# Performance work log

Hardware: AMD Instinct MI355X
Metric: run time of the kernel (lower is better)

## Reference

```python
import jax, jax.numpy as jnp
import numpy as np

N_NODES = 100000
N_EDGES = 1600000
F_NODE = 32
F_EDGE = 32
HID = 64
N_TGT = 32


def setup_inputs() -> dict:
    key = jax.random.key(0)
    ks = jax.random.split(key, 12)
    x = jax.random.normal(ks[0], (N_NODES, F_NODE), dtype=jnp.float32)
    edge_index = jax.random.randint(ks[1], (2, N_EDGES), 0, N_NODES, dtype=jnp.int64)
    edge_attr = jax.random.normal(ks[2], (N_EDGES, F_EDGE), dtype=jnp.float32)
    u = jax.random.normal(ks[3], (1, 8), dtype=jnp.float32)
    batch = jnp.zeros((N_NODES,), dtype=jnp.int64)
    s1 = 1.0 / np.sqrt(F_NODE + F_EDGE)
    s2 = 1.0 / np.sqrt(HID)
    s3 = 1.0 / np.sqrt(HID + F_NODE)
    W1a = jax.random.uniform(ks[4], (F_NODE + F_EDGE, HID), jnp.float32, -s1, s1)
    b1a = jax.random.uniform(ks[5], (HID,), jnp.float32, -s1, s1)
    W1b = jax.random.uniform(ks[6], (HID, HID), jnp.float32, -s2, s2)
    b1b = jax.random.uniform(ks[7], (HID,), jnp.float32, -s2, s2)
    W2a = jax.random.uniform(ks[8], (HID + F_NODE, HID), jnp.float32, -s3, s3)
    b2a = jax.random.uniform(ks[9], (HID,), jnp.float32, -s3, s3)
    W2b = jax.random.uniform(ks[10], (HID, N_TGT), jnp.float32, -s2, s2)
    b2b = jax.random.uniform(ks[11], (N_TGT,), jnp.float32, -s2, s2)
    return {"x": x, "edge_index": edge_index, "edge_attr": edge_attr, "u": u,
            "batch": batch, "W1a": W1a, "b1a": b1a, "W1b": W1b, "b1b": b1b,
            "W2a": W2a, "b2a": b2a, "W2b": W2b, "b2b": b2b}


def reference(x, edge_index, edge_attr, u, batch,
              W1a, b1a, W1b, b1b, W2a, b2a, W2b, b2b):
    row, col = edge_index[0], edge_index[1]
    n = x.shape[0]
    # gather source node features and concat with edge features -> edge MLP
    m = jnp.concatenate([x[col], edge_attr], axis=1)           # [E, F_NODE+F_EDGE]
    m = jax.nn.relu(m @ W1a + b1a) @ W1b + b1b                  # [E, HID]
    # scatter-mean back to destination nodes (row)
    summed = jax.ops.segment_sum(m, row, num_segments=n)        # [N, HID]
    counts = jax.ops.segment_sum(jnp.ones((m.shape[0],), m.dtype), row, num_segments=n)
    agg = summed / jnp.maximum(counts, 1.0)[:, None]
    h = jnp.concatenate([x, agg], axis=1)                       # [N, HID+F_NODE]
    out = jax.nn.relu(h @ W2a + b2a) @ W2b + b2b                # [N, N_TGT]
    return out
```

## Files before the change

kernel.cpp:

```cpp
#include <hip/hip_runtime.h>

#define NN 100000
#define NE 1600000
#define NB ((NN + 255) / 256)

typedef unsigned int uint32;
typedef unsigned short ushort16;
typedef float f32x4 __attribute__((ext_vector_type(4)));
typedef short bf16x8 __attribute__((ext_vector_type(8)));

__device__ __forceinline__ float bflo(uint32 u) { return __uint_as_float(u << 16); }
__device__ __forceinline__ float bfhi(uint32 u) { return __uint_as_float(u & 0xffff0000u); }
__device__ __forceinline__ uint32 bfbits(float v) { return (__float_as_uint(v) + 0x8000u) >> 16; }
__device__ __forceinline__ uint32 pack2(float a, float b) { return bfbits(a) | (bfbits(b) << 16); }

__device__ __forceinline__ int sigma_ch(int c) {
    return (((c >> 2) & 3) << 4) + (((c >> 4) & 3) << 2) + (c & 3);
}

__global__ __launch_bounds__(256) void k_hist_rank(const int* __restrict__ ei, int* __restrict__ deg,
                                                   int* __restrict__ rank, int E) {
    int e = blockIdx.x * 256 + threadIdx.x;
    if (e < E) rank[e] = atomicAdd(&deg[ei[e]], 1);
}

__global__ __launch_bounds__(256) void k_hist(const int* __restrict__ ei, int* __restrict__ deg, int E) {
    int e = blockIdx.x * 256 + threadIdx.x;
    if (e < E) atomicAdd(&deg[ei[e]], 1);
}

__global__ __launch_bounds__(256) void k_scan1(const int* __restrict__ deg, int* __restrict__ offs,
                                               int* __restrict__ bsums, int n) {
    __shared__ int s[256];
    int tid = threadIdx.x;
    int i = blockIdx.x * 256 + tid;
    int v = (i < n) ? deg[i] : 0;
    int acc = v;
    s[tid] = acc;
    __syncthreads();
    #pragma unroll
    for (int off = 1; off < 256; off <<= 1) {
        int t = (tid >= off) ? s[tid - off] : 0;
        __syncthreads();
        acc += t;
        s[tid] = acc;
        __syncthreads();
    }
    if (i < n) offs[i] = acc - v;
    if (tid == 255) bsums[blockIdx.x] = acc;
}

__global__ __launch_bounds__(512) void k_scan2(int* __restrict__ bsums, int nb) {
    __shared__ int s[512];
    int tid = threadIdx.x;
    int v = (tid < nb) ? bsums[tid] : 0;
    int acc = v;
    s[tid] = acc;
    __syncthreads();
    #pragma unroll
    for (int off = 1; off < 512; off <<= 1) {
        int t = (tid >= off) ? s[tid - off] : 0;
        __syncthreads();
        acc += t;
        s[tid] = acc;
        __syncthreads();
    }
    bsums[tid] = acc - v;
}

__global__ __launch_bounds__(256) void k_offs(int* __restrict__ offs, const int* __restrict__ bsums, int n) {
    int i = blockIdx.x * 256 + threadIdx.x;
    if (i < n) offs[i] += bsums[i >> 8];
}

__global__ __launch_bounds__(256) void k_sorted(const int* __restrict__ ei, const int* __restrict__ offs,
                                                const int* __restrict__ rank, int* __restrict__ sorted, int E) {
    int e = blockIdx.x * 256 + threadIdx.x;
    if (e >= E) return;
    sorted[offs[ei[e]] + rank[e]] = e;
}

__global__ __launch_bounds__(256) void k_prep(const float* __restrict__ W1b, const float* __restrict__ b1b,
                                              const float* __restrict__ W2a,
                                              float* __restrict__ Wc, float* __restrict__ bc, int perm) {
    int t = blockIdx.x * 256 + threadIdx.x;
    int r = t >> 6, c = t & 63;
    float a = 0.f;
    for (int k = 0; k < 64; ++k) a += W1b[r * 64 + k] * W2a[(32 + k) * 64 + c];
    int rs = perm ? sigma_ch(r) : r;
    Wc[rs * 64 + c] = a;
    if (t < 64) {
        float bacc = 0.f;
        for (int k = 0; k < 64; ++k) bacc += b1b[k] * W2a[(32 + k) * 64 + t];
        bc[t] = bacc;
    }
}

__global__ __launch_bounds__(256) void k_edge_fused(
    const int* __restrict__ ei, const float* __restrict__ ea, const float* __restrict__ x,
    const float* __restrict__ W1a, const float* __restrict__ b1a,
    const int* __restrict__ deg, const int* __restrict__ offs, const int* __restrict__ sorted,
    float* __restrict__ Sacc)
{
    __shared__ ushort16 sWtB[64 * 40];
    __shared__ ushort16 sWtA[64 * 40];
    for (int idx = threadIdx.x; idx < 2048; idx += 256) {
        int ch = idx & 63, k = idx >> 6;
        sWtB[ch * 40 + k] = (ushort16)bfbits(W1a[(32 + k) * 64 + ch]);
        sWtA[ch * 40 + k] = (ushort16)bfbits(W1a[k * 64 + ch]);
    }
    __syncthreads();

    int lane = threadIdx.x & 63;
    int wave = threadIdx.x >> 6;
    int en = lane & 15;
    int qq = lane >> 4;
    int node = blockIdx.x * 4 + wave;
    if (node >= NN) return;

    bf16x8 wB[4], wA[4];
    #pragma unroll
    for (int cc = 0; cc < 4; ++cc) {
        wB[cc] = *(const bf16x8*)&sWtB[(cc * 16 + en) * 40 + qq * 8];
        wA[cc] = *(const bf16x8*)&sWtA[(cc * 16 + en) * 40 + qq * 8];
    }
    f32x4 binit[4];
    #pragma unroll
    for (int cc = 0; cc < 4; ++cc) {
        float4 b = *(const float4*)(b1a + cc * 16 + qq * 4);
        binit[cc] = (f32x4){b.x, b.y, b.z, b.w};
    }

    int d = deg[node];
    int start = offs[node];

    f32x4 tot[4];
    #pragma unroll
    for (int cc = 0; cc < 4; ++cc) tot[cc] = (f32x4){0.f, 0.f, 0.f, 0.f};

    #pragma unroll 1
    for (int t0 = 0; t0 < d; t0 += 16) {
        int sidx = t0 + en;
        bool ok = sidx < d;
        union { uint4 u; bf16x8 v; } bea, bx;
        f32x4 acc[4];
        if (ok) {
            int e = sorted[start + sidx];
            int col = ei[NE + e];
            const float* ar = ea + (size_t)e * 32 + qq * 8;
            float4 a0 = *(const float4*)ar;
            float4 a1 = *(const float4*)(ar + 4);
            bea.u.x = pack2(a0.x, a0.y); bea.u.y = pack2(a0.z, a0.w);
            bea.u.z = pack2(a1.x, a1.y); bea.u.w = pack2(a1.z, a1.w);
            const float* xr = x + (size_t)col * 32 + qq * 8;
            float4 x0 = *(const float4*)xr;
            float4 x1 = *(const float4*)(xr + 4);
            bx.u.x = pack2(x0.x, x0.y); bx.u.y = pack2(x0.z, x0.w);
            bx.u.z = pack2(x1.x, x1.y); bx.u.w = pack2(x1.z, x1.w);
            #pragma unroll
            for (int cc = 0; cc < 4; ++cc) acc[cc] = binit[cc];
        } else {
            bea.u = make_uint4(0, 0, 0, 0);
            bx.u = make_uint4(0, 0, 0, 0);
            #pragma unroll
            for (int cc = 0; cc < 4; ++cc) acc[cc] = (f32x4){0.f, 0.f, 0.f, 0.f};
        }
        #pragma unroll
        for (int cc = 0; cc < 4; ++cc)
            acc[cc] = __builtin_amdgcn_mfma_f32_16x16x32_bf16(wB[cc], bea.v, acc[cc], 0, 0, 0);
        #pragma unroll
        for (int cc = 0; cc < 4; ++cc)
            acc[cc] = __builtin_amdgcn_mfma_f32_16x16x32_bf16(wA[cc], bx.v, acc[cc], 0, 0, 0);
        #pragma unroll
        for (int cc = 0; cc < 4; ++cc) {
            #pragma unroll
            for (int r = 0; r < 4; ++r)
                tot[cc][r] += fmaxf(acc[cc][r], 0.f);
        }
    }

    #pragma unroll
    for (int m = 1; m < 16; m <<= 1) {
        #pragma unroll
        for (int cc = 0; cc < 4; ++cc) {
            #pragma unroll
            for (int r = 0; r < 4; ++r)
                tot[cc][r] += __shfl_xor(tot[cc][r], m);
        }
    }
    if (en == 0) {
        float* sp = Sacc + (size_t)node * 64 + qq * 16;
        #pragma unroll
        for (int cc = 0; cc < 4; ++cc)
            *(float4*)(sp + cc * 4) = make_float4(tot[cc][0], tot[cc][1], tot[cc][2], tot[cc][3]);
    }
}

__global__ __launch_bounds__(256) void k_edge_atom(
    const float* __restrict__ x, const int* __restrict__ ei, const float* __restrict__ ea,
    const float* __restrict__ W1a, const float* __restrict__ b1a,
    float* __restrict__ Sacc, int E)
{
    __shared__ float sWB[32 * 64];
    __shared__ float sWA[32 * 64];
    __shared__ float sb[64];
    for (int t = threadIdx.x; t < 32 * 64; t += 256) {
        sWB[t] = W1a[32 * 64 + t];
        sWA[t] = W1a[t];
    }
    if (threadIdx.x < 64) sb[threadIdx.x] = b1a[threadIdx.x];
    __syncthreads();
    int e = blockIdx.x * 256 + threadIdx.x;
    if (e >= E) return;
    int row = ei[e];
    int col = ei[NE + e];
    float h[64];
    #pragma unroll
    for (int j = 0; j < 64; ++j) h[j] = sb[j];
    const float4* xrow = (const float4*)(x + (size_t)col * 32);
    #pragma unroll
    for (int k4 = 0; k4 < 8; ++k4) {
        float4 v = xrow[k4];
        float vv[4] = {v.x, v.y, v.z, v.w};
        #pragma unroll
        for (int c = 0; c < 4; ++c) {
            float val = vv[c];
            const float4* wr = (const float4*)&sWA[(k4 * 4 + c) * 64];
            #pragma unroll
            for (int j4 = 0; j4 < 16; ++j4) {
                float4 w = wr[j4];
                h[j4 * 4 + 0] += val * w.x; h[j4 * 4 + 1] += val * w.y;
                h[j4 * 4 + 2] += val * w.z; h[j4 * 4 + 3] += val * w.w;
            }
        }
    }
    const float4* earow = (const float4*)(ea + (size_t)e * 32);
    #pragma unroll
    for (int k4 = 0; k4 < 8; ++k4) {
        float4 v = earow[k4];
        float vv[4] = {v.x, v.y, v.z, v.w};
        #pragma unroll
        for (int c = 0; c < 4; ++c) {
            float val = vv[c];
            const float4* wr = (const float4*)&sWB[(k4 * 4 + c) * 64];
            #pragma unroll
            for (int j4 = 0; j4 < 16; ++j4) {
                float4 w = wr[j4];
                h[j4 * 4 + 0] += val * w.x; h[j4 * 4 + 1] += val * w.y;
                h[j4 * 4 + 2] += val * w.z; h[j4 * 4 + 3] += val * w.w;
            }
        }
    }
    float* srow = Sacc + (size_t)row * 64;
    #pragma unroll
    for (int j = 0; j < 64; ++j) atomicAdd(&srow[j], fmaxf(h[j], 0.f));
}

__global__ __launch_bounds__(256) void k_node(
    const float* __restrict__ x, const float* __restrict__ Sacc, const int* __restrict__ deg,
    const float* __restrict__ Wc, const float* __restrict__ bc,
    const float* __restrict__ W2a, const float* __restrict__ b2a,
    const float* __restrict__ W2b, const float* __restrict__ b2b,
    float* __restrict__ out, int N)
{
    __shared__ float sWc[64 * 64];
    __shared__ float sW2ax[32 * 64];
    __shared__ float sW2b[64 * 32];
    __shared__ float sbc2[64];
    __shared__ float sb2[64];
    __shared__ float sb2b_[32];
    for (int t = threadIdx.x; t < 64 * 64; t += 256) sWc[t] = Wc[t];
    for (int t = threadIdx.x; t < 32 * 64; t += 256) sW2ax[t] = W2a[t];
    for (int t = threadIdx.x; t < 64 * 32; t += 256) sW2b[t] = W2b[t];
    if (threadIdx.x < 64) {
        sbc2[threadIdx.x] = bc[threadIdx.x] + b2a[threadIdx.x];
        sb2[threadIdx.x] = b2a[threadIdx.x];
    }
    if (threadIdx.x < 32) sb2b_[threadIdx.x] = b2b[threadIdx.x];
    __syncthreads();

    int i = blockIdx.x * 256 + threadIdx.x;
    if (i >= N) return;
    int d = deg[i];
    float inv = (d > 0) ? 1.f / (float)d : 0.f;

    float h2[64];
    #pragma unroll
    for (int j = 0; j < 64; ++j) h2[j] = (d > 0) ? sbc2[j] : sb2[j];

    const float4* sp = (const float4*)(Sacc + (size_t)i * 64);
    #pragma unroll 2
    for (int k4 = 0; k4 < 16; ++k4) {
        float4 v = sp[k4];
        float vv[4] = {v.x * inv, v.y * inv, v.z * inv, v.w * inv};
        #pragma unroll
        for (int c = 0; c < 4; ++c) {
            float val = vv[c];
            const float4* wr = (const float4*)&sWc[(k4 * 4 + c) * 64];
            #pragma unroll
            for (int j4 = 0; j4 < 16; ++j4) {
                float4 w = wr[j4];
                h2[j4 * 4 + 0] += val * w.x; h2[j4 * 4 + 1] += val * w.y;
                h2[j4 * 4 + 2] += val * w.z; h2[j4 * 4 + 3] += val * w.w;
            }
        }
    }
    const float4* xrow = (const float4*)(x + (size_t)i * 32);
    #pragma unroll 2
    for (int k4 = 0; k4 < 8; ++k4) {
        float4 v = xrow[k4];
        float vv[4] = {v.x, v.y, v.z, v.w};
        #pragma unroll
        for (int c = 0; c < 4; ++c) {
            float val = vv[c];
            const float4* wr = (const float4*)&sW2ax[(k4 * 4 + c) * 64];
            #pragma unroll
            for (int j4 = 0; j4 < 16; ++j4) {
                float4 w = wr[j4];
                h2[j4 * 4 + 0] += val * w.x; h2[j4 * 4 + 1] += val * w.y;
                h2[j4 * 4 + 2] += val * w.z; h2[j4 * 4 + 3] += val * w.w;
            }
        }
    }
    #pragma unroll
    for (int j = 0; j < 64; ++j) h2[j] = fmaxf(h2[j], 0.f);

    float o[32];
    #pragma unroll
    for (int j = 0; j < 32; ++j) o[j] = sb2b_[j];
    #pragma unroll
    for (int k = 0; k < 64; ++k) {
        float val = h2[k];
        const float4* wr = (const float4*)&sW2b[k * 32];
        #pragma unroll
        for (int j4 = 0; j4 < 8; ++j4) {
            float4 w = wr[j4];
            o[j4 * 4 + 0] += val * w.x; o[j4 * 4 + 1] += val * w.y;
            o[j4 * 4 + 2] += val * w.z; o[j4 * 4 + 3] += val * w.w;
        }
    }
    float4* orow = (float4*)(out + (size_t)i * 32);
    #pragma unroll
    for (int q = 0; q < 8; ++q)
        orow[q] = make_float4(o[q * 4], o[q * 4 + 1], o[q * 4 + 2], o[q * 4 + 3]);
}

extern "C" void kernel_launch(void* const* d_in, const int* in_sizes, int n_in,
                              void* d_out, int out_size, void* d_ws, size_t ws_size,
                              hipStream_t stream) {
    const float* x   = (const float*)d_in[0];
    const int*   ei  = (const int*)d_in[1];
    const float* ea  = (const float*)d_in[2];
    const float* W1a = (const float*)d_in[5];
    const float* b1a = (const float*)d_in[6];
    const float* W1b = (const float*)d_in[7];
    const float* b1b = (const float*)d_in[8];
    const float* W2a = (const float*)d_in[9];
    const float* b2a = (const float*)d_in[10];
    const float* W2b = (const float*)d_in[11];
    const float* b2b = (const float*)d_in[12];
    float* out = (float*)d_out;

    char* p = (char*)d_ws;
    int* deg        = (int*)p;        p += (size_t)NN * 4;
    int* offs       = (int*)p;        p += (size_t)NN * 4;
    int* bsums      = (int*)p;        p += 2048;
    float* Wc       = (float*)p;      p += 4096 * 4;
    float* bc       = (float*)p;      p += 64 * 4;
    int* rank       = (int*)p;        p += (size_t)NE * 4;
    int* sorted     = (int*)p;        p += (size_t)NE * 4;
    float* Sacc     = (float*)p;      p += (size_t)NN * 64 * 4;
    size_t need     = (size_t)(p - (char*)d_ws);

    dim3 blk(256);
    bool primary = (ws_size >= need);

    if (primary) {
        hipMemsetAsync(deg, 0, (size_t)NN * 4, stream);
        hipLaunchKernelGGL(k_hist_rank, dim3((NE + 255) / 256), blk, 0, stream, ei, deg, rank, NE);
        hipLaunchKernelGGL(k_scan1, dim3(NB), blk, 0, stream, deg, offs, bsums, NN);
        hipLaunchKernelGGL(k_scan2, dim3(1), dim3(512), 0, stream, bsums, NB);
        hipLaunchKernelGGL(k_offs, dim3(NB), blk, 0, stream, offs, bsums, NN);
        hipLaunchKernelGGL(k_sorted, dim3((NE + 255) / 256), blk, 0, stream, ei, offs, rank, sorted, NE);
        hipLaunchKernelGGL(k_prep, dim3(16), blk, 0, stream, W1b, b1b, W2a, Wc, bc, 1);
        hipLaunchKernelGGL(k_edge_fused, dim3((NN + 3) / 4), blk, 0, stream,
                           ei, ea, x, W1a, b1a, deg, offs, sorted, Sacc);
        hipLaunchKernelGGL(k_node, dim3(NB), blk, 0, stream,
                           x, Sacc, deg, Wc, bc, W2a, b2a, W2b, b2b, out, NN);
    } else {
        hipMemsetAsync(deg, 0, (size_t)NN * 4, stream);
        hipMemsetAsync(Sacc, 0, (size_t)NN * 64 * 4, stream);
        hipLaunchKernelGGL(k_hist, dim3((NE + 255) / 256), blk, 0, stream, ei, deg, NE);
        hipLaunchKernelGGL(k_prep, dim3(16), blk, 0, stream, W1b, b1b, W2a, Wc, bc, 0);
        hipLaunchKernelGGL(k_edge_atom, dim3((NE + 255) / 256), blk, 0, stream,
                           x, ei, ea, W1a, b1a, Sacc, NE);
        hipLaunchKernelGGL(k_node, dim3(NB), blk, 0, stream,
                           x, Sacc, deg, Wc, bc, W2a, b2a, W2b, b2b, out, NN);
    }
}
```

Before: 333.0 us.

## Store edge id with source col during sort and prepack W1a MFMA fragments

The sort kernel now writes an (edge id, source column) pair per sorted slot, so the edge kernel no longer does a dependent gather of ei to find the column. W1a is converted to bf16 once in k_prep, stored in MFMA fragment layout, and loaded straight into registers. This drops the per-block shared-memory staging loop and its barrier. Out-of-range lanes now load a clamped valid slot, so loads are issued unconditionally. The trade-offs are a sorted array twice as large to write and read, and extra redundant loads for masked lanes.

Result: faster. 313.4 us (-5.9%).

```diff
diff --git a/kernel.cpp b/kernel.cpp
--- a/kernel.cpp
+++ b/kernel.cpp
@@ -74,15 +74,17 @@
 }
 
 __global__ __launch_bounds__(256) void k_sorted(const int* __restrict__ ei, const int* __restrict__ offs,
-                                                const int* __restrict__ rank, int* __restrict__ sorted, int E) {
+                                                const int* __restrict__ rank, int2* __restrict__ ecol, int E) {
     int e = blockIdx.x * 256 + threadIdx.x;
     if (e >= E) return;
-    sorted[offs[ei[e]] + rank[e]] = e;
+    int slot = offs[ei[e]] + rank[e];
+    ecol[slot] = make_int2(e, ei[E + e]);
 }
 
 __global__ __launch_bounds__(256) void k_prep(const float* __restrict__ W1b, const float* __restrict__ b1b,
-                                              const float* __restrict__ W2a,
-                                              float* __restrict__ Wc, float* __restrict__ bc, int perm) {
+                                              const float* __restrict__ W2a, const float* __restrict__ W1a,
+                                              float* __restrict__ Wc, float* __restrict__ bc,
+                                              uint4* __restrict__ wpack, int perm) {
     int t = blockIdx.x * 256 + threadIdx.x;
     int r = t >> 6, c = t & 63;
     float a = 0.f;
@@ -94,23 +96,29 @@
         for (int k = 0; k < 64; ++k) bacc += b1b[k] * W2a[(32 + k) * 64 + t];
         bc[t] = bacc;
     }
+    if (t < 512) {
+        int table = t >> 8;
+        int cc = (t >> 6) & 3;
+        int lane = t & 63;
+        int qq = lane >> 4, en = lane & 15;
+        int ch = cc * 16 + en;
+        uint32 w[4];
+        #pragma unroll
+        for (int j = 0; j < 4; ++j) {
+            int k0 = qq * 8 + j * 2;
+            int row0 = (table ? 0 : 32) + k0;
+            w[j] = pack2(W1a[row0 * 64 + ch], W1a[(row0 + 1) * 64 + ch]);
+        }
+        wpack[t] = make_uint4(w[0], w[1], w[2], w[3]);
+    }
 }
 
 __global__ __launch_bounds__(256) void k_edge_fused(
-    const int* __restrict__ ei, const float* __restrict__ ea, const float* __restrict__ x,
-    const float* __restrict__ W1a, const float* __restrict__ b1a,
-    const int* __restrict__ deg, const int* __restrict__ offs, const int* __restrict__ sorted,
+    const float* __restrict__ ea, const float* __restrict__ x,
+    const uint4* __restrict__ wpack, const float* __restrict__ b1a,
+    const int* __restrict__ deg, const int* __restrict__ offs, const int2* __restrict__ ecol,
     float* __restrict__ Sacc)
 {
-    __shared__ ushort16 sWtB[64 * 40];
-    __shared__ ushort16 sWtA[64 * 40];
-    for (int idx = threadIdx.x; idx < 2048; idx += 256) {
-        int ch = idx & 63, k = idx >> 6;
-        sWtB[ch * 40 + k] = (ushort16)bfbits(W1a[(32 + k) * 64 + ch]);
-        sWtA[ch * 40 + k] = (ushort16)bfbits(W1a[k * 64 + ch]);
-    }
-    __syncthreads();
-
     int lane = threadIdx.x & 63;
     int wave = threadIdx.x >> 6;
     int en = lane & 15;
@@ -118,11 +126,11 @@
     int node = blockIdx.x * 4 + wave;
     if (node >= NN) return;
 
-    bf16x8 wB[4], wA[4];
+    union { uint4 u; bf16x8 v; } wB[4], wA[4];
     #pragma unroll
     for (int cc = 0; cc < 4; ++cc) {
-        wB[cc] = *(const bf16x8*)&sWtB[(cc * 16 + en) * 40 + qq * 8];
-        wA[cc] = *(const bf16x8*)&sWtA[(cc * 16 + en) * 40 + qq * 8];
+        wB[cc].u = wpack[cc * 64 + lane];
+        wA[cc].u = wpack[256 + cc * 64 + lane];
     }
     f32x4 binit[4];
     #pragma unroll
@@ -142,19 +150,21 @@
     for (int t0 = 0; t0 < d; t0 += 16) {
         int sidx = t0 + en;
         bool ok = sidx < d;
+        int slot = start + (ok ? sidx : d - 1);
+        int2 ec = ecol[slot];
+
+        const float* ar = ea + (size_t)ec.x * 32 + qq * 8;
+        float4 a0 = *(const float4*)ar;
+        float4 a1 = *(const float4*)(ar + 4);
+        const float* xr = x + (size_t)ec.y * 32 + qq * 8;
+        float4 x0 = *(const float4*)xr;
+        float4 x1 = *(const float4*)(xr + 4);
+
         union { uint4 u; bf16x8 v; } bea, bx;
         f32x4 acc[4];
         if (ok) {
-            int e = sorted[start + sidx];
-            int col = ei[NE + e];
-            const float* ar = ea + (size_t)e * 32 + qq * 8;
-            float4 a0 = *(const float4*)ar;
-            float4 a1 = *(const float4*)(ar + 4);
             bea.u.x = pack2(a0.x, a0.y); bea.u.y = pack2(a0.z, a0.w);
             bea.u.z = pack2(a1.x, a1.y); bea.u.w = pack2(a1.z, a1.w);
-            const float* xr = x + (size_t)col * 32 + qq * 8;
-            float4 x0 = *(const float4*)xr;
-            float4 x1 = *(const float4*)(xr + 4);
             bx.u.x = pack2(x0.x, x0.y); bx.u.y = pack2(x0.z, x0.w);
             bx.u.z = pack2(x1.x, x1.y); bx.u.w = pack2(x1.z, x1.w);
             #pragma unroll
@@ -167,10 +177,10 @@
         }
         #pragma unroll
         for (int cc = 0; cc < 4; ++cc)
-            acc[cc] = __builtin_amdgcn_mfma_f32_16x16x32_bf16(wB[cc], bea.v, acc[cc], 0, 0, 0);
+            acc[cc] = __builtin_amdgcn_mfma_f32_16x16x32_bf16(wB[cc].v, bea.v, acc[cc], 0, 0, 0);
         #pragma unroll
         for (int cc = 0; cc < 4; ++cc)
-            acc[cc] = __builtin_amdgcn_mfma_f32_16x16x32_bf16(wA[cc], bx.v, acc[cc], 0, 0, 0);
+            acc[cc] = __builtin_amdgcn_mfma_f32_16x16x32_bf16(wA[cc].v, bx.v, acc[cc], 0, 0, 0);
         #pragma unroll
         for (int cc = 0; cc < 4; ++cc) {
             #pragma unroll
@@ -367,34 +377,36 @@
     int* bsums      = (int*)p;        p += 2048;
     float* Wc       = (float*)p;      p += 4096 * 4;
     float* bc       = (float*)p;      p += 64 * 4;
+    uint4* wpack    = (uint4*)p;      p += 512 * 16;
+    size_t off_fb   = (size_t)(p - (char*)d_ws);
     int* rank       = (int*)p;        p += (size_t)NE * 4;
-    int* sorted     = (int*)p;        p += (size_t)NE * 4;
+    int2* ecol      = (int2*)p;       p += (size_t)NE * 8;
     float* Sacc     = (float*)p;      p += (size_t)NN * 64 * 4;
     size_t need     = (size_t)(p - (char*)d_ws);
 
     dim3 blk(256);
-    bool primary = (ws_size >= need);
-
-    if (primary) {
+
+    if (ws_size >= need) {
         hipMemsetAsync(deg, 0, (size_t)NN * 4, stream);
         hipLaunchKernelGGL(k_hist_rank, dim3((NE + 255) / 256), blk, 0, stream, ei, deg, rank, NE);
         hipLaunchKernelGGL(k_scan1, dim3(NB), blk, 0, stream, deg, offs, bsums, NN);
         hipLaunchKernelGGL(k_scan2, dim3(1), dim3(512), 0, stream, bsums, NB);
         hipLaunchKernelGGL(k_offs, dim3(NB), blk, 0, stream, offs, bsums, NN);
-        hipLaunchKernelGGL(k_sorted, dim3((NE + 255) / 256), blk, 0, stream, ei, offs, rank, sorted, NE);
-        hipLaunchKernelGGL(k_prep, dim3(16), blk, 0, stream, W1b, b1b, W2a, Wc, bc, 1);
+        hipLaunchKernelGGL(k_sorted, dim3((NE + 255) / 256), blk, 0, stream, ei, offs, rank, ecol, NE);
+        hipLaunchKernelGGL(k_prep, dim3(16), blk, 0, stream, W1b, b1b, W2a, W1a, Wc, bc, wpack, 1);
         hipLaunchKernelGGL(k_edge_fused, dim3((NN + 3) / 4), blk, 0, stream,
-                           ei, ea, x, W1a, b1a, deg, offs, sorted, Sacc);
+                           ea, x, wpack, b1a, deg, offs, ecol, Sacc);
         hipLaunchKernelGGL(k_node, dim3(NB), blk, 0, stream,
                            x, Sacc, deg, Wc, bc, W2a, b2a, W2b, b2b, out, NN);
     } else {
+        float* Sacc_fb = (float*)((char*)d_ws + off_fb);
         hipMemsetAsync(deg, 0, (size_t)NN * 4, stream);
-        hipMemsetAsync(Sacc, 0, (size_t)NN * 64 * 4, stream);
+        hipMemsetAsync(Sacc_fb, 0, (size_t)NN * 64 * 4, stream);
         hipLaunchKernelGGL(k_hist, dim3((NE + 255) / 256), blk, 0, stream, ei, deg, NE);
-        hipLaunchKernelGGL(k_prep, dim3(16), blk, 0, stream, W1b, b1b, W2a, Wc, bc, 0);
+        hipLaunchKernelGGL(k_prep, dim3(16), blk, 0, stream, W1b, b1b, W2a, W1a, Wc, bc, wpack, 0);
         hipLaunchKernelGGL(k_edge_atom, dim3((NE + 255) / 256), blk, 0, stream,
-                           x, ei, ea, W1a, b1a, Sacc, NE);
+                           x, ei, ea, W1a, b1a, Sacc_fb, NE);
         hipLaunchKernelGGL(k_node, dim3(NB), blk, 0, stream,
-                           x, Sacc, deg, Wc, bc, W2a, b2a, W2b, b2b, out, NN);
-    }
-}
+                           x, Sacc_fb, deg, Wc, bc, W2a, b2a, W2b, b2b, out, NN);
+    }
+}
```
